# Performance work log

Hardware: AMD Instinct MI355X
Metric: run time of the kernel (lower is better)

## Reference

```python
import jax, jax.numpy as jnp
import numpy as np

B, C, H, W = 32, 256, 56, 56
HEADS, AG, GROUPS = 8, 49, 32
N = H * W
HEAD_DIM = C // HEADS
POOL = 7  # sqrt(agent_num)


def group_norm(x, w, b, groups=GROUPS, eps=1e-5):
    Bn, Cn, Hn, Wn = x.shape
    xg = x.reshape(Bn, groups, Cn // groups, Hn, Wn)
    m = xg.mean(axis=(2, 3, 4), keepdims=True)
    v = xg.var(axis=(2, 3, 4), keepdims=True)
    xn = ((xg - m) / jnp.sqrt(v + eps)).reshape(Bn, Cn, Hn, Wn)
    return xn * w[None, :, None, None] + b[None, :, None, None]


def conv1x1(x, w):
    # w: (out_ch, in_ch); 1x1 conv == per-pixel matmul
    return jnp.einsum('bchw,oc->bohw', x, w)


def setup_inputs() -> dict:
    key = jax.random.key(0)
    ks = jax.random.split(key, 16)
    s = 0.02
    d = {}
    d['x'] = jax.random.normal(ks[0], (B, C, H, W), jnp.float32)
    for i, p in enumerate(['q', 'k', 'v', 'p']):
        d[p + '_w'] = jax.random.normal(ks[1 + i], (C, C), jnp.float32) * s
        d[p + '_gw'] = jnp.ones((C,), jnp.float32)
        d[p + '_gb'] = jnp.zeros((C,), jnp.float32)
    d['dwc_w'] = jax.random.normal(ks[5], (C, 1, 3, 3), jnp.float32) * s
    d['dwc_b'] = jnp.zeros((C,), jnp.float32)
    d['an_bias'] = jax.random.normal(ks[6], (HEADS, AG, 7, 7), jnp.float32) * s
    d['na_bias'] = jax.random.normal(ks[7], (HEADS, AG, 7, 7), jnp.float32) * s
    d['ah_bias'] = jax.random.normal(ks[8], (1, HEADS, AG, W, 1), jnp.float32) * s
    d['aw_bias'] = jax.random.normal(ks[9], (1, HEADS, AG, 1, W), jnp.float32) * s
    d['ha_bias'] = jax.random.normal(ks[10], (1, HEADS, W, 1, AG), jnp.float32) * s
    d['wa_bias'] = jax.random.normal(ks[11], (1, HEADS, 1, W, AG), jnp.float32) * s
    return d


def reference(x, q_w, q_gw, q_gb, k_w, k_gw, k_gb, v_w, v_gw, v_gb,
              p_w, p_gw, p_gb, dwc_w, dwc_b,
              an_bias, na_bias, ah_bias, aw_bias, ha_bias, wa_bias):
    scale = HEAD_DIM ** -0.5
    q = group_norm(conv1x1(x, q_w), q_gw, q_gb)   # (B,C,H,W)
    k = group_norm(conv1x1(x, k_w), k_gw, k_gb)
    v = group_norm(conv1x1(x, v_w), v_gw, v_gb)

    # agent tokens: adaptive avg pool of q to 7x7 (56/7 = 8 exact blocks)
    at = q.reshape(B, C, POOL, H // POOL, POOL, W // POOL).mean(axis=(3, 5))  # (B,C,7,7)
    at = at.reshape(B, HEADS, HEAD_DIM, AG).transpose(0, 1, 3, 2)             # (B,h,a,d)

    qh = q.reshape(B, HEADS, HEAD_DIM, N).transpose(0, 1, 3, 2)  # (B,h,N,d)
    kh = k.reshape(B, HEADS, HEAD_DIM, N).transpose(0, 1, 3, 2)
    vh = v.reshape(B, HEADS, HEAD_DIM, N).transpose(0, 1, 3, 2)

    # stage 1: agents attend to keys/values
    pb1 = jax.image.resize(an_bias, (HEADS, AG, H, W), 'bilinear').reshape(1, HEADS, AG, N)
    pb2 = (ah_bias + aw_bias).reshape(1, HEADS, AG, N)
    agent_attn = jax.nn.softmax(
        jnp.einsum('bhad,bhnd->bhan', at * scale, kh) + pb1 + pb2, axis=-1)
    agent_v = jnp.einsum('bhan,bhnd->bhad', agent_attn, vh)  # (B,h,a,d)

    # stage 2: queries attend to agents
    ab1 = jax.image.resize(na_bias, (HEADS, AG, H, W), 'bilinear').reshape(1, HEADS, AG, N).transpose(0, 1, 3, 2)
    ab2 = (ha_bias + wa_bias).reshape(1, HEADS, N, AG)
    q_attn = jax.nn.softmax(
        jnp.einsum('bhnd,bhad->bhna', qh * scale, at) + ab1 + ab2, axis=-1)
    xo = jnp.einsum('bhna,bhad->bhnd', q_attn, agent_v)      # (B,h,N,d)
    xo = xo.transpose(0, 2, 1, 3).reshape(B, N, C)

    # depthwise conv residual on value feature map
    dw = jax.lax.conv_general_dilated(
        v, dwc_w, (1, 1), 'SAME', feature_group_count=C,
        dimension_numbers=('NCHW', 'OIHW', 'NCHW')) + dwc_b[None, :, None, None]
    xo = xo + dw.transpose(0, 2, 3, 1).reshape(B, N, C)

    xo = xo.transpose(0, 2, 1).reshape(B, C, H, W)
    return group_norm(conv1x1(xo, p_w), p_gw, p_gb)
```

## Files before the change

kernel.cpp:

```cpp
#include <hip/hip_runtime.h>
#include <hip/hip_bf16.h>
#include <math.h>

#define BB      32
#define CC      256
#define HDIM    56
#define NPIX    3136
#define NHEADS  8
#define HD      32
#define AG      49
#define NGROUPS 32
#define CPG     8
#define SCALE   0.17677669529663687f

typedef short s16x8 __attribute__((ext_vector_type(8)));
typedef float f32x4 __attribute__((ext_vector_type(4)));
typedef unsigned int u32;

#define GLL16(g, l)                                                        \
  __builtin_amdgcn_global_load_lds(                                        \
      (const u32 __attribute__((address_space(1)))*)(g),                   \
      (u32 __attribute__((address_space(3)))*)(l), 16, 0, 0)

__global__ __launch_bounds__(256) void convert_w_kernel(
    const float* __restrict__ q, const float* __restrict__ k,
    const float* __restrict__ v, const float* __restrict__ p,
    __bf16* __restrict__ w) {
  const int i = blockIdx.x * 256 + threadIdx.x;
  const int z = blockIdx.y;
  const float* src = z == 0 ? q : z == 1 ? k : z == 2 ? v : p;
  w[(size_t)z * 65536 + i] = (__bf16)src[i];
}

__global__ __launch_bounds__(256) void transpose_kernel(
    const float* __restrict__ X, __bf16* __restrict__ Xt) {
  const int nt = blockIdx.x, ct = blockIdx.y, b = blockIdx.z;
  __shared__ __bf16 T[64][72];
  const int t = threadIdx.x;
  const int c0 = ct * 64, n0 = nt * 64;
  {
    const int c = t >> 2;
    const float* src = X + ((size_t)b * CC + c0 + c) * NPIX + n0;
#pragma unroll
    for (int j = 0; j < 4; ++j) {
      const int col = (t & 3) * 16 + j * 4;
      const float4 v = *(const float4*)&src[col];
      T[c][col + 0] = (__bf16)v.x;
      T[c][col + 1] = (__bf16)v.y;
      T[c][col + 2] = (__bf16)v.z;
      T[c][col + 3] = (__bf16)v.w;
    }
  }
  __syncthreads();
  {
    const int n = t >> 2;
    const int cl0 = (t & 3) * 16;
    __bf16* dst = Xt + ((size_t)b * NPIX + n0 + n) * CC + c0 + cl0;
    union { __bf16 e[16]; uint4 u[2]; } buf;
#pragma unroll
    for (int j = 0; j < 16; ++j) buf.e[j] = T[cl0 + j][n];
    *(uint4*)(dst + 0) = buf.u[0];
    *(uint4*)(dst + 8) = buf.u[1];
  }
}

template <typename T>
__global__ __launch_bounds__(256) void gemm_kernel(
    const __bf16* __restrict__ W, const __bf16* __restrict__ Xt,
    T* __restrict__ O0, T* __restrict__ O1, T* __restrict__ O2) {
  __shared__ __bf16 As[128 * 32];
  __shared__ __bf16 Bs[64 * 32];
  const int bx = blockIdx.x;
  const int by = blockIdx.y;
  const int b = blockIdx.z;
  const int t = threadIdx.x;
  const int o0 = by * 128;

  const int ar0 = t >> 2, G = t & 3;
  const int sa0 = G ^ ((ar0 >> 1) & 3);
  const int ar1 = 64 + ar0;
  const int sa1 = G ^ ((ar1 >> 1) & 3);
  const char* wbase = (const char*)W;
  const char* xbase = (const char*)(Xt + ((size_t)b * NPIX + bx * 64) * CC);
  const size_t ga0 = (size_t)(o0 + ar0) * 512 + sa0 * 16;
  const size_t ga1 = (size_t)(o0 + ar1) * 512 + sa1 * 16;
  const size_t gb0 = (size_t)ar0 * 512 + sa0 * 16;
  char* lA0 = (char*)As + t * 16;
  char* lA1 = (char*)As + 4096 + t * 16;
  char* lB0 = (char*)Bs + t * 16;

  const int wv = t >> 6, ln = t & 63;
  const int wm = wv >> 1, wn = wv & 1;
  const int l15 = ln & 15, g4 = ln >> 4;

  const f32x4 zz = {0.f, 0.f, 0.f, 0.f};
  f32x4 acc[4][2];
#pragma unroll
  for (int mi = 0; mi < 4; ++mi)
#pragma unroll
    for (int ni = 0; ni < 2; ++ni) acc[mi][ni] = zz;

  for (int k0 = 0; k0 < 256; k0 += 32) {
    GLL16(wbase + ga0 + k0 * 2, lA0);
    GLL16(wbase + ga1 + k0 * 2, lA1);
    GLL16(xbase + gb0 + k0 * 2, lB0);
    __syncthreads();
    s16x8 fa[4], fb[2];
#pragma unroll
    for (int mi = 0; mi < 4; ++mi) {
      const int r = wm * 64 + mi * 16 + l15;
      const int rx = (r & 6) << 3;
      const char* p = (const char*)As + r * 64;
      union { uint2 u[2]; s16x8 v; } tmp;
      tmp.u[0] = *(const uint2*)(p + ((g4 << 3) ^ rx));
      tmp.u[1] = *(const uint2*)(p + (((g4 + 4) << 3) ^ rx));
      fa[mi] = tmp.v;
    }
#pragma unroll
    for (int ni = 0; ni < 2; ++ni) {
      const int r = wn * 32 + ni * 16 + l15;
      const int rx = (r & 6) << 3;
      const char* p = (const char*)Bs + r * 64;
      union { uint2 u[2]; s16x8 v; } tmp;
      tmp.u[0] = *(const uint2*)(p + ((g4 << 3) ^ rx));
      tmp.u[1] = *(const uint2*)(p + (((g4 + 4) << 3) ^ rx));
      fb[ni] = tmp.v;
    }
#pragma unroll
    for (int mi = 0; mi < 4; ++mi)
#pragma unroll
      for (int ni = 0; ni < 2; ++ni)
        acc[mi][ni] = __builtin_amdgcn_mfma_f32_16x16x32_bf16(
            fa[mi], fb[ni], acc[mi][ni], 0, 0, 0);
    __syncthreads();
  }
#pragma unroll
  for (int mi = 0; mi < 4; ++mi) {
    const int ob = o0 + wm * 64 + mi * 16 + g4 * 4;
#pragma unroll
    for (int ni = 0; ni < 2; ++ni) {
      const int n = bx * 64 + wn * 32 + ni * 16 + l15;
#pragma unroll
      for (int r = 0; r < 4; ++r) {
        const int oo = ob + r;
        T* dst = (oo < 256) ? O0 : (oo < 512) ? O1 : O2;
        dst[((size_t)b * CC + (oo & 255)) * NPIX + n] = (T)acc[mi][ni][r];
      }
    }
  }
}

__global__ __launch_bounds__(256) void qkvstat_kernel(
    const __bf16* __restrict__ qkv, const float* __restrict__ qgw,
    const float* __restrict__ qgb, const float* __restrict__ kgw,
    const float* __restrict__ kgb, const float* __restrict__ vgw,
    const float* __restrict__ vgb, float* __restrict__ sc,
    float* __restrict__ sh) {
  const int zg = blockIdx.x, b = blockIdx.y;
  const int t = threadIdx.x, w = t >> 6, ln = t & 63;
  __shared__ float Ss[8], Qs[8];
  __shared__ float st[2];
#pragma unroll
  for (int j = 0; j < 2; ++j) {
    const int ch = zg * 8 + w * 2 + j;
    const int z = ch >> 8, c = ch & 255;
    const __bf16* row =
        qkv + ((size_t)z * BB * CC + (size_t)b * CC + c) * NPIX;
    float S = 0.f, Q = 0.f;
    for (int i = ln; i < 392; i += 64) {
      union { uint4 u; __bf16 e[8]; } v;
      v.u = *(const uint4*)&row[i * 8];
#pragma unroll
      for (int e = 0; e < 8; ++e) {
        const float f = (float)v.e[e];
        S += f;
        Q += f * f;
      }
    }
#pragma unroll
    for (int off = 32; off > 0; off >>= 1) {
      S += __shfl_down(S, off);
      Q += __shfl_down(Q, off);
    }
    if (ln == 0) {
      Ss[w * 2 + j] = S;
      Qs[w * 2 + j] = Q;
    }
  }
  __syncthreads();
  if (t == 0) {
    float S = 0.f, Q = 0.f;
#pragma unroll
    for (int i = 0; i < 8; ++i) {
      S += Ss[i];
      Q += Qs[i];
    }
    const float m = S / 25088.f;
    const float var = Q / 25088.f - m * m;
    st[0] = m;
    st[1] = rsqrtf(var + 1e-5f);
  }
  __syncthreads();
  if (t < 8) {
    const int ch = zg * 8 + t;
    const int z = ch >> 8, c = ch & 255;
    const float gw = z == 0 ? qgw[c] : z == 1 ? kgw[c] : vgw[c];
    const float gb = z == 0 ? qgb[c] : z == 1 ? kgb[c] : vgb[c];
    const float s = gw * st[1];
    sc[(size_t)b * 768 + ch] = s;
    sh[(size_t)b * 768 + ch] = gb - st[0] * s;
  }
}

__global__ __launch_bounds__(256) void gn_kernel(
    const float* __restrict__ in, const float* __restrict__ gw,
    const float* __restrict__ gb, float* __restrict__ out) {
  const int g = blockIdx.x, b = blockIdx.y;
  const float* p = in + ((size_t)b * CC + g * CPG) * NPIX;
  float* q = out + ((size_t)b * CC + g * CPG) * NPIX;
  const int tid = threadIdx.x;
  const int M4 = CPG * NPIX / 4;
  const float4* p4 = (const float4*)p;
  float4* q4 = (float4*)q;
  float4 r[25];
  float s = 0.f, ss = 0.f;
#pragma unroll
  for (int j = 0; j < 25; ++j) {
    const int i = tid + j * 256;
    if (i < M4) {
      const float4 v = p4[i];
      r[j] = v;
      s += v.x + v.y + v.z + v.w;
      ss += v.x * v.x + v.y * v.y + v.z * v.z + v.w * v.w;
    }
  }
#pragma unroll
  for (int off = 32; off > 0; off >>= 1) {
    s += __shfl_down(s, off);
    ss += __shfl_down(ss, off);
  }
  __shared__ float wsum[4], wsq[4], stat[2];
  const int wv = tid >> 6, lnn = tid & 63;
  if (lnn == 0) { wsum[wv] = s; wsq[wv] = ss; }
  __syncthreads();
  if (tid == 0) {
    float S = wsum[0] + wsum[1] + wsum[2] + wsum[3];
    float SS = wsq[0] + wsq[1] + wsq[2] + wsq[3];
    const float inv_m = 1.f / (CPG * NPIX);
    float mean = S * inv_m;
    float var = SS * inv_m - mean * mean;
    stat[0] = mean;
    stat[1] = rsqrtf(var + 1e-5f);
  }
  __syncthreads();
  const float mean = stat[0], inv = stat[1];
#pragma unroll
  for (int j = 0; j < 25; ++j) {
    const int i = tid + j * 256;
    if (i < M4) {
      const int ch = g * CPG + i / (NPIX / 4);
      const float w = gw[ch] * inv, bia = gb[ch];
      float4 v = r[j];
      v.x = (v.x - mean) * w + bia;
      v.y = (v.y - mean) * w + bia;
      v.z = (v.z - mean) * w + bia;
      v.w = (v.w - mean) * w + bia;
      q4[i] = v;
    }
  }
}

__global__ __launch_bounds__(64) void pool_kernel(
    const __bf16* __restrict__ q, const float* __restrict__ sc,
    const float* __restrict__ sh, float* __restrict__ at) {
  const int bc = blockIdx.x;
  const int a = threadIdx.x;
  if (a >= AG) return;
  const int b = bc >> 8, c = bc & 255;
  const int py = a / 7, px = a % 7;
  const __bf16* p = q + (size_t)bc * NPIX + (py * 8) * HDIM + px * 8;
  float s = 0.f;
#pragma unroll
  for (int y = 0; y < 8; ++y)
#pragma unroll
    for (int x = 0; x < 8; ++x) s += (float)p[y * HDIM + x];
  at[(size_t)bc * AG + a] =
      s * (1.f / 64.f) * sc[(size_t)b * 768 + c] + sh[(size_t)b * 768 + c];
}

__device__ __forceinline__ float bilin7(const float* __restrict__ src, int y,
                                        int x) {
  float sy = fminf(fmaxf((y + 0.5f) * 0.125f - 0.5f, 0.f), 6.f);
  float sx = fminf(fmaxf((x + 0.5f) * 0.125f - 0.5f, 0.f), 6.f);
  int y0 = (int)sy, x0 = (int)sx;
  int y1 = min(y0 + 1, 6), x1 = min(x0 + 1, 6);
  float fy = sy - y0, fx = sx - x0;
  return (1.f - fy) * ((1.f - fx) * src[y0 * 7 + x0] + fx * src[y0 * 7 + x1]) +
         fy * ((1.f - fx) * src[y1 * 7 + x0] + fx * src[y1 * 7 + x1]);
}

__global__ __launch_bounds__(256) void bias1_kernel(
    const float* __restrict__ an, const float* __restrict__ ah,
    const float* __restrict__ aw, float* __restrict__ pbt) {
  const int ha = blockIdx.x;
  const int h = ha / AG, a = ha % AG;
  const float* src = an + (size_t)ha * 49;
  const float* ahp = ah + (size_t)ha * HDIM;
  const float* awp = aw + (size_t)ha * HDIM;
  for (int n = threadIdx.x; n < NPIX; n += 256) {
    const int y = n / HDIM, x = n % HDIM;
    pbt[((size_t)h * NPIX + n) * 64 + a] = bilin7(src, y, x) + ahp[y] + awp[x];
  }
}

__global__ __launch_bounds__(256) void fill_kernel(float* __restrict__ p,
                                                   int n4) {
  const int i = blockIdx.x * 256 + threadIdx.x;
  if (i < n4) {
    float4 v = make_float4(-1e9f, -1e9f, -1e9f, -1e9f);
    *(float4*)&p[i * 4] = v;
  }
}

__global__ __launch_bounds__(256) void bias2_kernel(
    const float* __restrict__ na, const float* __restrict__ hab,
    const float* __restrict__ wab, float* __restrict__ ab2) {
  const int ha = blockIdx.x;
  const int h = ha / AG, a = ha % AG;
  const float* src = na + (size_t)ha * 49;
  for (int n = threadIdx.x; n < NPIX; n += 256) {
    const int y = n / HDIM, x = n % HDIM;
    ab2[((size_t)h * NPIX + n) * 64 + a] =
        bilin7(src, y, x) + hab[((size_t)h * HDIM + y) * AG + a] +
        wab[((size_t)h * HDIM + x) * AG + a];
  }
}

__global__ __launch_bounds__(256) void tr_k_kernel(
    const __bf16* __restrict__ K, __bf16* __restrict__ Kt) {
  const int nt = blockIdx.x, h = blockIdx.y, b = blockIdx.z;
  const int n0 = nt * 64;
  __shared__ __bf16 T[32][72];
  const int t = threadIdx.x;
  {
    const int d = t >> 3, c8 = (t & 7) * 8;
    *(uint4*)&T[d][c8] =
        *(const uint4*)&K[((size_t)(b * CC + h * HD + d)) * NPIX + n0 + c8];
  }
  __syncthreads();
  {
    const int n = t >> 2, d0 = (t & 3) * 8;
    union { __bf16 e[8]; uint4 u; } buf;
#pragma unroll
    for (int j = 0; j < 8; ++j) buf.e[j] = T[d0 + j][n];
    *(uint4*)&Kt[((size_t)(b * NHEADS + h) * NPIX + n0 + n) * HD + d0] = buf.u;
  }
}

__global__ __launch_bounds__(256) void stage1_kernel(
    const __bf16* __restrict__ Kt, const __bf16* __restrict__ V,
    const float* __restrict__ at, const float* __restrict__ pbt,
    const float* __restrict__ sc, const float* __restrict__ sh,
    float* __restrict__ av) {
  const int bh = blockIdx.x;
  const int b = bh >> 3, h = bh & 7;
  const int t = threadIdx.x;
  const int w = t >> 6, ln = t & 63;
  const int l15 = ln & 15, g4 = ln >> 4;

  __shared__ float atraw[64][33];
  __shared__ float sck_s[32], shk_s[32];
  __shared__ float cb_s[64];
  __shared__ __bf16 at_s[64][40];
  __shared__ __bf16 Es[4][64][40];
  __shared__ float avs[4][64][33];
  __shared__ float Ls[4][64];

  if (t < 32) {
    const size_t si = (size_t)b * 768 + 256 + h * HD + t;
    sck_s[t] = sc[si];
    shk_s[t] = sh[si];
  }
  for (int i = t; i < 64 * 32; i += 256) {
    const int d = i >> 6, a = i & 63;
    atraw[a][d] =
        (a < AG) ? at[((size_t)b * CC + h * HD + d) * AG + a] * SCALE : 0.f;
  }
  __syncthreads();
  if (t < 64) {
    float s = 0.f;
#pragma unroll
    for (int d = 0; d < HD; ++d) {
      const float v = atraw[t][d];
      s += v * shk_s[d];
      at_s[t][d] = (__bf16)(v * sck_s[d]);
    }
    cb_s[t] = s;
  }
  __syncthreads();

  s16x8 fa[4];
  float4 cbv[4];
#pragma unroll
  for (int mt = 0; mt < 4; ++mt) {
    fa[mt] = *(const s16x8*)&at_s[mt * 16 + l15][g4 * 8];
    cbv[mt] = *(const float4*)&cb_s[mt * 16 + g4 * 4];
  }

  const __bf16* Ktb = Kt + (size_t)bh * NPIX * HD;
  const __bf16* Vcb = V + ((size_t)b * CC + h * HD) * NPIX;
  const float* pbh = pbt + (size_t)h * NPIX * 64;

  const f32x4 zz = {0.f, 0.f, 0.f, 0.f};
  f32x4 avacc[4][2];
#pragma unroll
  for (int mt = 0; mt < 4; ++mt) {
    avacc[mt][0] = zz;
    avacc[mt][1] = zz;
  }
  float lsum[4][4] = {};

  for (int ct = w; ct < 98; ct += 4) {
    const int nc0 = ct * 32;
    f32x4 c0[4], c1[4];
    {
      const s16x8 kf0 =
          *(const s16x8*)&Ktb[(size_t)(nc0 + l15) * HD + g4 * 8];
      const s16x8 kf1 =
          *(const s16x8*)&Ktb[(size_t)(nc0 + 16 + l15) * HD + g4 * 8];
#pragma unroll
      for (int mt = 0; mt < 4; ++mt) {
        c0[mt] = __builtin_amdgcn_mfma_f32_16x16x32_bf16(fa[mt], kf0, zz, 0, 0, 0);
        c1[mt] = __builtin_amdgcn_mfma_f32_16x16x32_bf16(fa[mt], kf1, zz, 0, 0, 0);
      }
    }
#pragma unroll
    for (int mt = 0; mt < 4; ++mt) {
      const int a0 = mt * 16 + g4 * 4;
      {
        const float4 bi =
            *(const float4*)&pbh[(size_t)(nc0 + l15) * 64 + a0];
        const float e0 = __expf(c0[mt][0] + bi.x + cbv[mt].x);
        const float e1 = __expf(c0[mt][1] + bi.y + cbv[mt].y);
        const float e2 = __expf(c0[mt][2] + bi.z + cbv[mt].z);
        const float e3 = __expf(c0[mt][3] + bi.w + cbv[mt].w);
        lsum[mt][0] += e0; lsum[mt][1] += e1;
        lsum[mt][2] += e2; lsum[mt][3] += e3;
        Es[w][a0 + 0][l15] = (__bf16)e0;
        Es[w][a0 + 1][l15] = (__bf16)e1;
        Es[w][a0 + 2][l15] = (__bf16)e2;
        Es[w][a0 + 3][l15] = (__bf16)e3;
      }
      {
        const float4 bi =
            *(const float4*)&pbh[(size_t)(nc0 + 16 + l15) * 64 + a0];
        const float e0 = __expf(c1[mt][0] + bi.x + cbv[mt].x);
        const float e1 = __expf(c1[mt][1] + bi.y + cbv[mt].y);
        const float e2 = __expf(c1[mt][2] + bi.z + cbv[mt].z);
        const float e3 = __expf(c1[mt][3] + bi.w + cbv[mt].w);
        lsum[mt][0] += e0; lsum[mt][1] += e1;
        lsum[mt][2] += e2; lsum[mt][3] += e3;
        Es[w][a0 + 0][16 + l15] = (__bf16)e0;
        Es[w][a0 + 1][16 + l15] = (__bf16)e1;
        Es[w][a0 + 2][16 + l15] = (__bf16)e2;
        Es[w][a0 + 3][16 + l15] = (__bf16)e3;
      }
    }
    asm volatile("s_waitcnt lgkmcnt(0)" ::: "memory");
    const s16x8 vf0 =
        *(const s16x8*)&Vcb[(size_t)(l15) * NPIX + nc0 + g4 * 8];
    const s16x8 vf1 =
        *(const s16x8*)&Vcb[(size_t)(16 + l15) * NPIX + nc0 + g4 * 8];
#pragma unroll
    for (int mt = 0; mt < 4; ++mt) {
      const s16x8 ef = *(const s16x8*)&Es[w][mt * 16 + l15][g4 * 8];
      avacc[mt][0] =
          __builtin_amdgcn_mfma_f32_16x16x32_bf16(ef, vf0, avacc[mt][0], 0, 0, 0);
      avacc[mt][1] =
          __builtin_amdgcn_mfma_f32_16x16x32_bf16(ef, vf1, avacc[mt][1], 0, 0, 0);
    }
  }

#pragma unroll
  for (int mt = 0; mt < 4; ++mt)
#pragma unroll
    for (int r = 0; r < 4; ++r) {
      float v = lsum[mt][r];
      v += __shfl_xor(v, 1);
      v += __shfl_xor(v, 2);
      v += __shfl_xor(v, 4);
      v += __shfl_xor(v, 8);
      if (l15 == 0) Ls[w][mt * 16 + g4 * 4 + r] = v;
    }
#pragma unroll
  for (int mt = 0; mt < 4; ++mt)
#pragma unroll
    for (int dt = 0; dt < 2; ++dt)
#pragma unroll
      for (int r = 0; r < 4; ++r)
        avs[w][mt * 16 + g4 * 4 + r][dt * 16 + l15] = avacc[mt][dt][r];
  __syncthreads();
  for (int i = t; i < AG * HD; i += 256) {
    const int a = i >> 5, d = i & 31;
    const float L = Ls[0][a] + Ls[1][a] + Ls[2][a] + Ls[3][a];
    const float s = avs[0][a][d] + avs[1][a][d] + avs[2][a][d] + avs[3][a][d];
    const size_t si = (size_t)b * 768 + 512 + h * HD + d;
    av[((size_t)bh * AG + a) * HD + d] = (s / L) * sc[si] + sh[si];
  }
}

__global__ __launch_bounds__(256) void stage2_kernel(
    const __bf16* __restrict__ Qt, const float* __restrict__ at,
    const float* __restrict__ av, const float* __restrict__ ab2,
    const float* __restrict__ sc, const float* __restrict__ sh,
    float* __restrict__ XO) {
  const int s = blockIdx.x;
  const int bh = blockIdx.y;
  const int b = bh >> 3, h = bh & 7;
  const int t = threadIdx.x;
  const int w = t >> 6, ln = t & 63;
  const int l15 = ln & 15, g4 = ln >> 4;

  __shared__ float atraw[64][33];
  __shared__ float scq_s[32], shq_s[32];
  __shared__ float cb2_s[64];
  __shared__ __bf16 atb[64][40];
  __shared__ __bf16 avbT[32][72];
  __shared__ __bf16 Es[4][16][72];
  __shared__ float Os[4][16][33];

  if (t < 32) {
    const size_t si = (size_t)b * 768 + h * HD + t;
    scq_s[t] = sc[si];
    shq_s[t] = sh[si];
  }
  for (int i = t; i < 64 * 32; i += 256) {
    const int d = i >> 6, a = i & 63;
    atraw[a][d] =
        (a < AG) ? at[((size_t)b * CC + h * HD + d) * AG + a] * SCALE : 0.f;
  }
  for (int i = t; i < 32 * 64; i += 256) {
    const int d = i >> 6, a = i & 63;
    const float v = (a < AG) ? av[((size_t)bh * AG + a) * HD + d] : 0.f;
    avbT[d][a] = (__bf16)v;
  }
  __syncthreads();
  if (t < 64) {
    float s2 = 0.f;
#pragma unroll
    for (int d = 0; d < HD; ++d) {
      const float v = atraw[t][d];
      s2 += v * shq_s[d];
      atb[t][d] = (__bf16)(v * scq_s[d]);
    }
    cb2_s[t] = s2;
  }
  __syncthreads();

  s16x8 at_fB[4];
  float q2b[4];
#pragma unroll
  for (int atile = 0; atile < 4; ++atile) {
    at_fB[atile] = *(const s16x8*)&atb[atile * 16 + l15][g4 * 8];
    q2b[atile] = cb2_s[atile * 16 + l15];
  }
  s16x8 av_fB[2][2];
#pragma unroll
  for (int dt = 0; dt < 2; ++dt)
#pragma unroll
    for (int ks = 0; ks < 2; ++ks)
      av_fB[dt][ks] = *(const s16x8*)&avbT[dt * 16 + l15][ks * 32 + g4 * 8];

  const __bf16* Qtb = Qt + (size_t)bh * NPIX * HD;
  const float* abh = ab2 + (size_t)h * NPIX * 64;
  float* Ob = XO + ((size_t)b * CC + h * HD) * NPIX;
  const f32x4 zz = {0.f, 0.f, 0.f, 0.f};
  const int nbase = s * 784;

  for (int ct = w; ct < 49; ct += 4) {
    const int n0 = nbase + ct * 16;
    const s16x8 qf = *(const s16x8*)&Qtb[(size_t)(n0 + l15) * HD + g4 * 8];
    f32x4 c[4];
#pragma unroll
    for (int atile = 0; atile < 4; ++atile)
      c[atile] = __builtin_amdgcn_mfma_f32_16x16x32_bf16(qf, at_fB[atile], zz, 0, 0, 0);
    float Lr[4];
#pragma unroll
    for (int r = 0; r < 4; ++r) {
      const int n = n0 + g4 * 4 + r;
      const float* brow = &abh[(size_t)n * 64];
      float es[4];
#pragma unroll
      for (int atile = 0; atile < 4; ++atile) {
        const float e = __expf(c[atile][r] + brow[atile * 16 + l15] + q2b[atile]);
        es[atile] = e;
        Es[w][g4 * 4 + r][atile * 16 + l15] = (__bf16)e;
      }
      float sr = (es[0] + es[1]) + (es[2] + es[3]);
      sr += __shfl_xor(sr, 1);
      sr += __shfl_xor(sr, 2);
      sr += __shfl_xor(sr, 4);
      sr += __shfl_xor(sr, 8);
      Lr[r] = sr;
    }
    asm volatile("s_waitcnt lgkmcnt(0)" ::: "memory");
    const s16x8 ef0 = *(const s16x8*)&Es[w][l15][g4 * 8];
    const s16x8 ef1 = *(const s16x8*)&Es[w][l15][32 + g4 * 8];
    f32x4 o0 = __builtin_amdgcn_mfma_f32_16x16x32_bf16(ef0, av_fB[0][0], zz, 0, 0, 0);
    o0 = __builtin_amdgcn_mfma_f32_16x16x32_bf16(ef1, av_fB[0][1], o0, 0, 0, 0);
    f32x4 o1 = __builtin_amdgcn_mfma_f32_16x16x32_bf16(ef0, av_fB[1][0], zz, 0, 0, 0);
    o1 = __builtin_amdgcn_mfma_f32_16x16x32_bf16(ef1, av_fB[1][1], o1, 0, 0, 0);
#pragma unroll
    for (int r = 0; r < 4; ++r) {
      const float inv = 1.f / Lr[r];
      Os[w][g4 * 4 + r][l15] = o0[r] * inv;
      Os[w][g4 * 4 + r][16 + l15] = o1[r] * inv;
    }
    asm volatile("s_waitcnt lgkmcnt(0)" ::: "memory");
#pragma unroll
    for (int it = 0; it < 8; ++it) {
      const int d = it * 4 + g4;
      Ob[(size_t)d * NPIX + n0 + l15] = Os[w][l15][d];
    }
  }
}

__global__ __launch_bounds__(256) void dwconv_kernel(
    const __bf16* __restrict__ V, const float* __restrict__ sc,
    const float* __restrict__ sh, const float* __restrict__ w,
    const float* __restrict__ bias, float* __restrict__ XO) {
  const int bc = blockIdx.x;
  const int c = bc % CC;
  const int b = bc >> 8;
  const int tid = threadIdx.x;
  __shared__ float T[58][60];
  float* Tf = &T[0][0];
  for (int i = tid; i < 58 * 60; i += 256) Tf[i] = 0.f;
  __syncthreads();
  const size_t si = (size_t)b * 768 + 512 + c;
  const float scl = sc[si], shf = sh[si];
  const __bf16* src = V + (size_t)bc * NPIX;
  for (int i = tid; i < 392; i += 256) {
    const int y = i / 7, x8 = (i % 7) * 8;
    union { uint4 u; __bf16 e[8]; } raw;
    raw.u = *(const uint4*)&src[y * HDIM + x8];
#pragma unroll
    for (int j = 0; j < 8; ++j)
      T[y + 1][x8 + 1 + j] = (float)raw.e[j] * scl + shf;
  }
  __syncthreads();
  float k[9];
#pragma unroll
  for (int i = 0; i < 9; ++i) k[i] = w[c * 9 + i];
  const float bb = bias[c];
  float* dst = XO + (size_t)bc * NPIX;
  for (int n = tid; n < NPIX; n += 256) {
    const int y = n / HDIM, x = n % HDIM;
    const float s = bb +
        k[0] * T[y][x]     + k[1] * T[y][x + 1]     + k[2] * T[y][x + 2] +
        k[3] * T[y + 1][x] + k[4] * T[y + 1][x + 1] + k[5] * T[y + 1][x + 2] +
        k[6] * T[y + 2][x] + k[7] * T[y + 2][x + 1] + k[8] * T[y + 2][x + 2];
    dst[n] += s;
  }
}

extern "C" void kernel_launch(void* const* d_in, const int* in_sizes, int n_in,
                              void* d_out, int out_size, void* d_ws,
                              size_t ws_size, hipStream_t stream) {
  const float* x     = (const float*)d_in[0];
  const float* q_w   = (const float*)d_in[1];
  const float* q_gw  = (const float*)d_in[2];
  const float* q_gb  = (const float*)d_in[3];
  const float* k_w   = (const float*)d_in[4];
  const float* k_gw  = (const float*)d_in[5];
  const float* k_gb  = (const float*)d_in[6];
  const float* v_w   = (const float*)d_in[7];
  const float* v_gw  = (const float*)d_in[8];
  const float* v_gb  = (const float*)d_in[9];
  const float* p_w   = (const float*)d_in[10];
  const float* p_gw  = (const float*)d_in[11];
  const float* p_gb  = (const float*)d_in[12];
  const float* dwc_w = (const float*)d_in[13];
  const float* dwc_b = (const float*)d_in[14];
  const float* an_b  = (const float*)d_in[15];
  const float* na_b  = (const float*)d_in[16];
  const float* ah_b  = (const float*)d_in[17];
  const float* aw_b  = (const float*)d_in[18];
  const float* ha_b  = (const float*)d_in[19];
  const float* wa_b  = (const float*)d_in[20];
  float* out = (float*)d_out;

  const size_t SZ_FEAT = (size_t)BB * CC * NPIX;
  const size_t SZ_AT   = (size_t)BB * CC * AG;
  const size_t SZ_PBT  = (size_t)NHEADS * NPIX * 64;
  const size_t SZ_AV   = (size_t)BB * NHEADS * AG * HD;
  const size_t SZ_SC   = (size_t)BB * 768;
  const size_t need =
      3 * SZ_FEAT * sizeof(__bf16) +
      (SZ_FEAT + SZ_AT + 2 * SZ_PBT + SZ_AV + 2 * SZ_SC) * sizeof(float) +
      1024 * 256 * sizeof(__bf16);
  if (ws_size < need) return;

  __bf16* qbf = (__bf16*)d_ws;
  __bf16* kbf = qbf + SZ_FEAT;
  __bf16* vbf = kbf + SZ_FEAT;
  float* xo  = (float*)(vbf + SZ_FEAT);
  float* at  = xo + SZ_FEAT;
  float* pbt = at + SZ_AT;
  float* ab2 = pbt + SZ_PBT;
  float* av  = ab2 + SZ_PBT;
  __bf16* wbf = (__bf16*)(av + SZ_AV);
  float* sc = (float*)(wbf + 1024 * 256);
  float* sh = sc + SZ_SC;

  __bf16* xbf = (__bf16*)d_out;
  __bf16* Kt  = (__bf16*)((char*)d_out + SZ_FEAT * 2);
  __bf16* Qt  = Kt;

  const dim3 ggrid(NGROUPS, BB);
  const dim3 tgrid(49, 4, BB);

  convert_w_kernel<<<dim3(256, 4), 256, 0, stream>>>(q_w, k_w, v_w, p_w, wbf);
  transpose_kernel<<<tgrid, 256, 0, stream>>>(x, xbf);
  gemm_kernel<__bf16><<<dim3(49, 6, BB), 256, 0, stream>>>(wbf, xbf, qbf, kbf,
                                                           vbf);
  qkvstat_kernel<<<dim3(96, BB), 256, 0, stream>>>(qbf, q_gw, q_gb, k_gw,
                                                   k_gb, v_gw, v_gb, sc, sh);

  pool_kernel<<<BB * CC, 64, 0, stream>>>(qbf, sc, sh, at);
  hipMemsetAsync(pbt, 0, SZ_PBT * sizeof(float), stream);
  bias1_kernel<<<NHEADS * AG, 256, 0, stream>>>(an_b, ah_b, aw_b, pbt);
  fill_kernel<<<(int)(SZ_PBT / 4 + 255) / 256, 256, 0, stream>>>(
      ab2, (int)(SZ_PBT / 4));
  bias2_kernel<<<NHEADS * AG, 256, 0, stream>>>(na_b, ha_b, wa_b, ab2);

  tr_k_kernel<<<dim3(49, NHEADS, BB), 256, 0, stream>>>(kbf, Kt);
  stage1_kernel<<<BB * NHEADS, 256, 0, stream>>>(Kt, vbf, at, pbt, sc, sh, av);

  tr_k_kernel<<<dim3(49, NHEADS, BB), 256, 0, stream>>>(qbf, Qt);
  stage2_kernel<<<dim3(4, BB * NHEADS), 256, 0, stream>>>(Qt, at, av, ab2, sc,
                                                          sh, xo);
  dwconv_kernel<<<BB * CC, 256, 0, stream>>>(vbf, sc, sh, dwc_w, dwc_b, xo);

  transpose_kernel<<<tgrid, 256, 0, stream>>>(xo, xbf);
  gemm_kernel<float><<<dim3(49, 2, BB), 256, 0, stream>>>(wbf + 768 * 256,
                                                          xbf, xo, xo, xo);
  gn_kernel<<<ggrid, 256, 0, stream>>>(xo, p_gw, p_gb, out);
}
```

Measured before the change: 495.4 us.

## Load GEMM MFMA fragments directly from global memory instead of staging through LDS

The 1x1-conv GEMM kernel no longer copies tiles of the weights and activations into shared memory with global_load_lds followed by barriers. Each lane now reads its 16-byte bf16 MFMA operand fragments straight from global memory, and the K loop is fully unrolled so the compiler can issue loads early. This removes the LDS traffic and the two __syncthreads per K step. In exchange, waves that share the same A or B rows read them redundantly from L1/L2, and the strided row loads may coalesce less well.

```diff
diff --git a/kernel.cpp b/kernel.cpp
--- a/kernel.cpp
+++ b/kernel.cpp
@@ -17,11 +17,6 @@
 typedef float f32x4 __attribute__((ext_vector_type(4)));
 typedef unsigned int u32;
 
-#define GLL16(g, l)                                                        \
-  __builtin_amdgcn_global_load_lds(                                        \
-      (const u32 __attribute__((address_space(1)))*)(g),                   \
-      (u32 __attribute__((address_space(3)))*)(l), 16, 0, 0)
-
 __global__ __launch_bounds__(256) void convert_w_kernel(
     const float* __restrict__ q, const float* __restrict__ k,
     const float* __restrict__ v, const float* __restrict__ p,
@@ -68,31 +63,19 @@
 __global__ __launch_bounds__(256) void gemm_kernel(
     const __bf16* __restrict__ W, const __bf16* __restrict__ Xt,
     T* __restrict__ O0, T* __restrict__ O1, T* __restrict__ O2) {
-  __shared__ __bf16 As[128 * 32];
-  __shared__ __bf16 Bs[64 * 32];
   const int bx = blockIdx.x;
   const int by = blockIdx.y;
   const int b = blockIdx.z;
   const int t = threadIdx.x;
   const int o0 = by * 128;
-
-  const int ar0 = t >> 2, G = t & 3;
-  const int sa0 = G ^ ((ar0 >> 1) & 3);
-  const int ar1 = 64 + ar0;
-  const int sa1 = G ^ ((ar1 >> 1) & 3);
-  const char* wbase = (const char*)W;
-  const char* xbase = (const char*)(Xt + ((size_t)b * NPIX + bx * 64) * CC);
-  const size_t ga0 = (size_t)(o0 + ar0) * 512 + sa0 * 16;
-  const size_t ga1 = (size_t)(o0 + ar1) * 512 + sa1 * 16;
-  const size_t gb0 = (size_t)ar0 * 512 + sa0 * 16;
-  char* lA0 = (char*)As + t * 16;
-  char* lA1 = (char*)As + 4096 + t * 16;
-  char* lB0 = (char*)Bs + t * 16;
-
   const int wv = t >> 6, ln = t & 63;
   const int wm = wv >> 1, wn = wv & 1;
   const int l15 = ln & 15, g4 = ln >> 4;
 
+  const __bf16* A0 = W + (size_t)(o0 + wm * 64 + l15) * 256 + g4 * 8;
+  const __bf16* B0 = Xt +
+      ((size_t)b * NPIX + bx * 64 + wn * 32 + l15) * 256 + g4 * 8;
+
   const f32x4 zz = {0.f, 0.f, 0.f, 0.f};
   f32x4 acc[4][2];
 #pragma unroll
@@ -100,39 +83,21 @@
 #pragma unroll
     for (int ni = 0; ni < 2; ++ni) acc[mi][ni] = zz;
 
+#pragma unroll
   for (int k0 = 0; k0 < 256; k0 += 32) {
-    GLL16(wbase + ga0 + k0 * 2, lA0);
-    GLL16(wbase + ga1 + k0 * 2, lA1);
-    GLL16(xbase + gb0 + k0 * 2, lB0);
-    __syncthreads();
     s16x8 fa[4], fb[2];
 #pragma unroll
-    for (int mi = 0; mi < 4; ++mi) {
-      const int r = wm * 64 + mi * 16 + l15;
-      const int rx = (r & 6) << 3;
-      const char* p = (const char*)As + r * 64;
-      union { uint2 u[2]; s16x8 v; } tmp;
-      tmp.u[0] = *(const uint2*)(p + ((g4 << 3) ^ rx));
-      tmp.u[1] = *(const uint2*)(p + (((g4 + 4) << 3) ^ rx));
-      fa[mi] = tmp.v;
-    }
-#pragma unroll
-    for (int ni = 0; ni < 2; ++ni) {
-      const int r = wn * 32 + ni * 16 + l15;
-      const int rx = (r & 6) << 3;
-      const char* p = (const char*)Bs + r * 64;
-      union { uint2 u[2]; s16x8 v; } tmp;
-      tmp.u[0] = *(const uint2*)(p + ((g4 << 3) ^ rx));
-      tmp.u[1] = *(const uint2*)(p + (((g4 + 4) << 3) ^ rx));
-      fb[ni] = tmp.v;
-    }
+    for (int mi = 0; mi < 4; ++mi)
+      fa[mi] = *(const s16x8*)(A0 + (size_t)mi * 16 * 256 + k0);
+#pragma unroll
+    for (int ni = 0; ni < 2; ++ni)
+      fb[ni] = *(const s16x8*)(B0 + (size_t)ni * 16 * 256 + k0);
 #pragma unroll
     for (int mi = 0; mi < 4; ++mi)
 #pragma unroll
       for (int ni = 0; ni < 2; ++ni)
         acc[mi][ni] = __builtin_amdgcn_mfma_f32_16x16x32_bf16(
             fa[mi], fb[ni], acc[mi][ni], 0, 0, 0);
-    __syncthreads();
   }
 #pragma unroll
   for (int mi = 0; mi < 4; ++mi) {
```

New measurement: 643.1 us. +29.8%, slower.
